# Optimization experiments

Hardware: AMD Instinct MI355X
Metric: run time of the kernel (lower is better)

Reference implementation:

```python
import jax, jax.numpy as jnp
import numpy as np

DELTA_VAR = 0.5
DELTA_DIST = 1.5
LOSS_WEIGHT = 1.0
L_MAX = 17  # segment ids 0..16 (0 = background)
EPS = 1e-12


def setup_inputs() -> dict:
    key = jax.random.key(0)
    k1, k2 = jax.random.split(key)
    B, D, H, W = 16, 16, 288, 512
    emb = jax.random.normal(k1, (B, D, H, W), dtype=jnp.float32)
    seg = jax.random.randint(k2, (B, 1, H, W), 0, L_MAX, dtype=jnp.int64)
    return {"input": emb, "target": seg}


def _per_image_losses(e, s):
    # e: [D, N] float, s: [N] int labels in [0, L_MAX)
    D, N = e.shape
    et = e.T  # [N, D]
    cnt = jax.ops.segment_sum(jnp.ones((N,), e.dtype), s, num_segments=L_MAX)  # [L]
    sums = jax.ops.segment_sum(et, s, num_segments=L_MAX)                      # [L, D]
    present = (cnt > 0) & (jnp.arange(L_MAX) != 0)
    num_lanes = jnp.sum(present).astype(e.dtype)
    means = sums / jnp.maximum(cnt, 1.0)[:, None]                              # [L, D]

    # variance (pull) term: per-pixel distance to own-label centroid
    diff = et - means[s]                                                       # [N, D]
    nrm = jnp.sqrt(jnp.maximum(jnp.sum(diff * diff, axis=1), EPS))             # [N]
    term = jax.nn.relu(nrm - DELTA_VAR) ** 2
    per_label = jax.ops.segment_sum(term, s, num_segments=L_MAX) / jnp.maximum(cnt, 1.0)
    var_l = jnp.sum(jnp.where(present, per_label, 0.0)) / jnp.maximum(num_lanes, 1.0)
    var_l = jnp.where(num_lanes > 0, var_l, 0.0)

    # distance (push) term: pairwise centroid distances among present lanes
    d = means[:, None, :] - means[None, :, :]                                  # [L, L, D]
    sumsq = jnp.sum(d * d, axis=2)                                             # [L, L]
    pair_mask = present[:, None] & present[None, :] & ~jnp.eye(L_MAX, dtype=bool)
    dist = jnp.sqrt(jnp.where(pair_mask, sumsq, 1.0))
    push = jnp.sum(jnp.where(pair_mask, jax.nn.relu(DELTA_DIST - dist) ** 2, 0.0))
    denom = jnp.maximum(num_lanes * (num_lanes - 1.0), 1.0)
    dist_l = jnp.where(num_lanes > 1, push / denom / 2.0, 0.0)
    return var_l, dist_l


def reference(input, target):
    B, D, H, W = input.shape
    N = H * W
    emb = input.reshape(B, D, N)
    seg = target.reshape(B, N).astype(jnp.int32)
    var_l, dist_l = jax.vmap(_per_image_losses)(emb, seg)
    loss = (jnp.sum(var_l) + jnp.sum(dist_l)) / B
    return loss * LOSS_WEIGHT
```

## Files before the change

kernel.cpp:

```cpp
#include <hip/hip_runtime.h>

#define BB   16
#define DD   16
#define NN   (288*512)
#define LL   17
#define TPB  256
#define PB   96
#define QB   (NN/4/PB)
#define PBV  144
#define NREP 8

#define FSCALE 32768.0f
#define INV_FSCALE (1.0f/32768.0f)


__global__ __launch_bounds__(TPB) void k_accum(const float* __restrict__ emb,
                                               const int* __restrict__ seg,
                                               int* __restrict__ acc) {
    __shared__ int tab[NREP * 289];
    const int tid  = threadIdx.x;
    const int b    = blockIdx.y;
    const int blk  = blockIdx.x;
    const int dgrp = tid >> 6;
    const int j    = tid & 63;
    int* trep = tab + (j & (NREP - 1)) * 289;

    for (int i = tid; i < NREP * 289; i += TPB) tab[i] = 0;

    const float* embb = emb + (size_t)b * DD * NN;
    const int*   segb = seg + (size_t)b * NN;
    const float* r0 = embb + (size_t)(dgrp * 4 + 0) * NN;
    const float* r1 = embb + (size_t)(dgrp * 4 + 1) * NN;
    const float* r2 = embb + (size_t)(dgrp * 4 + 2) * NN;
    const float* r3 = embb + (size_t)(dgrp * 4 + 3) * NN;
    const int q0 = blk * QB;
    __syncthreads();

#pragma unroll
    for (int it = 0; it < QB / 64; ++it) {
        const int n = (q0 + it * 64 + j) * 4;
        const int4   s4 = *(const int4*)(segb + n);
        const float4 e0 = *(const float4*)(r0 + n);
        const float4 e1 = *(const float4*)(r1 + n);
        const float4 e2 = *(const float4*)(r2 + n);
        const float4 e3 = *(const float4*)(r3 + n);
        const int ch = dgrp * 4;
        const int o0 = s4.x * 17 + ch;
        const int o1 = s4.y * 17 + ch;
        const int o2 = s4.z * 17 + ch;
        const int o3 = s4.w * 17 + ch;
        atomicAdd(trep + o0 + 0, __float2int_rn(e0.x * FSCALE));
        atomicAdd(trep + o0 + 1, __float2int_rn(e1.x * FSCALE));
        atomicAdd(trep + o0 + 2, __float2int_rn(e2.x * FSCALE));
        atomicAdd(trep + o0 + 3, __float2int_rn(e3.x * FSCALE));
        atomicAdd(trep + o1 + 0, __float2int_rn(e0.y * FSCALE));
        atomicAdd(trep + o1 + 1, __float2int_rn(e1.y * FSCALE));
        atomicAdd(trep + o1 + 2, __float2int_rn(e2.y * FSCALE));
        atomicAdd(trep + o1 + 3, __float2int_rn(e3.y * FSCALE));
        atomicAdd(trep + o2 + 0, __float2int_rn(e0.z * FSCALE));
        atomicAdd(trep + o2 + 1, __float2int_rn(e1.z * FSCALE));
        atomicAdd(trep + o2 + 2, __float2int_rn(e2.z * FSCALE));
        atomicAdd(trep + o2 + 3, __float2int_rn(e3.z * FSCALE));
        atomicAdd(trep + o3 + 0, __float2int_rn(e0.w * FSCALE));
        atomicAdd(trep + o3 + 1, __float2int_rn(e1.w * FSCALE));
        atomicAdd(trep + o3 + 2, __float2int_rn(e2.w * FSCALE));
        atomicAdd(trep + o3 + 3, __float2int_rn(e3.w * FSCALE));
        if (dgrp == 0) {
            atomicAdd(trep + s4.x * 17 + 16, 1);
            atomicAdd(trep + s4.y * 17 + 16, 1);
            atomicAdd(trep + s4.z * 17 + 16, 1);
            atomicAdd(trep + s4.w * 17 + 16, 1);
        }
    }
    __syncthreads();

    for (int i = tid; i < 289; i += TPB) {
        int v = 0;
#pragma unroll
        for (int r = 0; r < NREP; ++r) v += tab[r * 289 + i];
        atomicAdd(acc + b * 289 + i, v);
    }
}

__global__ __launch_bounds__(TPB) void k_var(const float* __restrict__ emb,
                                             const int* __restrict__ seg,
                                             const int* __restrict__ acc,
                                             float* __restrict__ vpart) {
    __shared__ float m[289];
    __shared__ float wl[17];
    __shared__ float wsum[TPB / 64];
    const int tid = threadIdx.x;
    const int b = blockIdx.y;

    for (int i = tid; i < 289; i += TPB) {
        const int raw = acc[b * 289 + i];
        m[i] = (i % 17 == 16) ? (float)raw : (float)raw * INV_FSCALE;
    }
    __syncthreads();
    for (int i = tid; i < 272; i += TPB) {
        const int l = i >> 4, d = i & 15;
        m[l * 17 + d] /= fmaxf(m[l * 17 + 16], 1.f);
    }
    __syncthreads();

    int nl = 0;
#pragma unroll
    for (int l = 1; l < LL; ++l) nl += (m[l * 17 + 16] > 0.f) ? 1 : 0;
    const float nlf = (float)nl;
    if (tid < LL) {
        const bool pres = (tid != 0) && (m[tid * 17 + 16] > 0.f);
        wl[tid] = pres ? 1.f / (fmaxf(m[tid * 17 + 16], 1.f) * fmaxf(nlf, 1.f) * (float)BB)
                       : 0.f;
    }
    __syncthreads();

    const float* embb = emb + (size_t)b * DD * NN;
    const int*   segb = seg + (size_t)b * NN;

    const int n = blockIdx.x * (TPB * 4) + tid * 4;
    const int4 s4 = *(const int4*)(segb + n);
    const int o0 = s4.x * 17, o1 = s4.y * 17, o2 = s4.z * 17, o3 = s4.w * 17;
    float ss0 = 0.f, ss1 = 0.f, ss2 = 0.f, ss3 = 0.f;
#pragma unroll
    for (int d = 0; d < DD; ++d) {
        const float4 e = *(const float4*)(embb + (size_t)d * NN + n);
        const float d0 = e.x - m[o0 + d]; ss0 += d0 * d0;
        const float d1 = e.y - m[o1 + d]; ss1 += d1 * d1;
        const float d2 = e.z - m[o2 + d]; ss2 += d2 * d2;
        const float d3 = e.w - m[o3 + d]; ss3 += d3 * d3;
    }
    float accl = 0.f, t;
    t = fmaxf(sqrtf(fmaxf(ss0, 1e-12f)) - 0.5f, 0.f); accl += t * t * wl[s4.x];
    t = fmaxf(sqrtf(fmaxf(ss1, 1e-12f)) - 0.5f, 0.f); accl += t * t * wl[s4.y];
    t = fmaxf(sqrtf(fmaxf(ss2, 1e-12f)) - 0.5f, 0.f); accl += t * t * wl[s4.z];
    t = fmaxf(sqrtf(fmaxf(ss3, 1e-12f)) - 0.5f, 0.f); accl += t * t * wl[s4.w];

    if (blockIdx.x == 0 && nl > 1) {
        float push = 0.f;
        for (int p = tid; p < 289; p += TPB) {
            const int i = p / 17, jj = p % 17;
            if (i != jj && i > 0 && jj > 0 && m[i*17+16] > 0.f && m[jj*17+16] > 0.f) {
                float ss = 0.f;
#pragma unroll
                for (int d = 0; d < DD; ++d) {
                    const float df = m[i*17+d] - m[jj*17+d];
                    ss += df * df;
                }
                const float u = fmaxf(1.5f - sqrtf(ss), 0.f);
                push += u * u;
            }
        }
        accl += push / (fmaxf(nlf * (nlf - 1.f), 1.f) * 2.f * (float)BB);
    }

#pragma unroll
    for (int off = 32; off; off >>= 1) accl += __shfl_down(accl, off, 64);
    if ((tid & 63) == 0) wsum[tid >> 6] = accl;
    __syncthreads();
    if (tid == 0)
        vpart[(size_t)b * PBV + blockIdx.x] = wsum[0] + wsum[1] + wsum[2] + wsum[3];
}

__global__ __launch_bounds__(TPB) void k_final(const float* __restrict__ vpart,
                                               float* __restrict__ out) {
    __shared__ float ws4[TPB / 64];
    float v = 0.f;
    for (int i = threadIdx.x; i < BB * PBV; i += TPB) v += vpart[i];
#pragma unroll
    for (int off = 32; off; off >>= 1) v += __shfl_down(v, off, 64);
    if ((threadIdx.x & 63) == 0) ws4[threadIdx.x >> 6] = v;
    __syncthreads();
    if (threadIdx.x == 0) out[0] = ws4[0] + ws4[1] + ws4[2] + ws4[3];
}

extern "C" void kernel_launch(void* const* d_in, const int* in_sizes, int n_in,
                              void* d_out, int out_size, void* d_ws, size_t ws_size,
                              hipStream_t stream) {
    const float* emb = (const float*)d_in[0];
    const int*   seg = (const int*)d_in[1];
    float* out = (float*)d_out;

    int*   acc   = (int*)d_ws;
    float* vpart = (float*)(acc + BB * 289);

    hipMemsetAsync(acc, 0, (size_t)BB * 289 * sizeof(int), stream);

    k_accum<<<dim3(PB, BB), TPB, 0, stream>>>(emb, seg, acc);
    k_var  <<<dim3(PBV, BB), TPB, 0, stream>>>(emb, seg, acc, vpart);
    k_final<<<1, TPB, 0, stream>>>(vpart, out);
}
```

Measured before the change: 246.2 us.

## Fuse accumulate, variance and final reduce into one cooperative kernel with grid sync

Adds a cooperative kernel that runs centroid accumulation, a grid-wide sync, the variance/push pass and the final reduction in one launch. Each block processes the same pixel range in both phases, so the second read of the embeddings may hit the large last-level cache instead of HBM. Launch overhead for three kernels is also removed. The cost is lower occupancy (512 blocks of 256 threads), grid-sync latency, and dependence on cooperative launch support, with the old three-kernel path kept as a fallback.

```diff
diff --git a/kernel.cpp b/kernel.cpp
--- a/kernel.cpp
+++ b/kernel.cpp
@@ -1,29 +1,46 @@
 #include <hip/hip_runtime.h>
+#include <hip/hip_cooperative_groups.h>
+
+namespace cg = cooperative_groups;
 
 #define BB   16
 #define DD   16
 #define NN   (288*512)
 #define LL   17
 #define TPB  256
+#define NREP 8
+
+#define NBLK 512
+#define BPI  (NBLK/BB)
+#define PXB  (NN/BPI)
+#define QB   (PXB/4)
+
 #define PB   96
-#define QB   (NN/4/PB)
+#define QBF  (NN/4/PB)
 #define PBV  144
-#define NREP 8
 
 #define FSCALE 32768.0f
 #define INV_FSCALE (1.0f/32768.0f)
 
 
-__global__ __launch_bounds__(TPB) void k_accum(const float* __restrict__ emb,
-                                               const int* __restrict__ seg,
-                                               int* __restrict__ acc) {
-    __shared__ int tab[NREP * 289];
+__global__ __launch_bounds__(TPB, 2) void k_fused(const float* __restrict__ emb,
+                                                  const int* __restrict__ seg,
+                                                  int* __restrict__ acc,
+                                                  float* __restrict__ vpart,
+                                                  float* __restrict__ out) {
+    __shared__ int   tab[NREP * 289];
+    __shared__ float m[289];
+    __shared__ float wl[LL];
+    __shared__ float wsum[TPB / 64];
+
+    cg::grid_group grid = cg::this_grid();
+
     const int tid  = threadIdx.x;
-    const int b    = blockIdx.y;
-    const int blk  = blockIdx.x;
+    const int bid  = blockIdx.x;
+    const int b    = bid / BPI;
+    const int blk  = bid % BPI;
     const int dgrp = tid >> 6;
     const int j    = tid & 63;
-    int* trep = tab + (j & (NREP - 1)) * 289;
 
     for (int i = tid; i < NREP * 289; i += TPB) tab[i] = 0;
 
@@ -34,9 +51,9 @@
     const float* r2 = embb + (size_t)(dgrp * 4 + 2) * NN;
     const float* r3 = embb + (size_t)(dgrp * 4 + 3) * NN;
     const int q0 = blk * QB;
-    __syncthreads();
-
-#pragma unroll
+    int* trep = tab + (j & (NREP - 1)) * 289;
+    __syncthreads();
+
     for (int it = 0; it < QB / 64; ++it) {
         const int n = (q0 + it * 64 + j) * 4;
         const int4   s4 = *(const int4*)(segb + n);
@@ -73,6 +90,155 @@
         }
     }
     __syncthreads();
+    for (int i = tid; i < 289; i += TPB) {
+        int v = 0;
+#pragma unroll
+        for (int r = 0; r < NREP; ++r) v += tab[r * 289 + i];
+        atomicAdd(acc + b * 289 + i, v);
+    }
+
+    grid.sync();
+
+    for (int i = tid; i < 289; i += TPB) {
+        const int raw = acc[b * 289 + i];
+        m[i] = (i % 17 == 16) ? (float)raw : (float)raw * INV_FSCALE;
+    }
+    __syncthreads();
+    for (int i = tid; i < 272; i += TPB) {
+        const int l = i >> 4, d = i & 15;
+        m[l * 17 + d] /= fmaxf(m[l * 17 + 16], 1.f);
+    }
+    __syncthreads();
+
+    int nl = 0;
+#pragma unroll
+    for (int l = 1; l < LL; ++l) nl += (m[l * 17 + 16] > 0.f) ? 1 : 0;
+    const float nlf = (float)nl;
+    if (tid < LL) {
+        const bool pres = (tid != 0) && (m[tid * 17 + 16] > 0.f);
+        wl[tid] = pres ? 1.f / (fmaxf(m[tid * 17 + 16], 1.f) * fmaxf(nlf, 1.f) * (float)BB)
+                       : 0.f;
+    }
+    __syncthreads();
+
+    float accl = 0.f;
+    const int base = blk * PXB;
+    for (int p = tid * 4; p < PXB; p += TPB * 4) {
+        const int n = base + p;
+        const int4 s4 = *(const int4*)(segb + n);
+        const int o0 = s4.x * 17, o1 = s4.y * 17, o2 = s4.z * 17, o3 = s4.w * 17;
+        float ss0 = 0.f, ss1 = 0.f, ss2 = 0.f, ss3 = 0.f;
+#pragma unroll
+        for (int d = 0; d < DD; ++d) {
+            const float4 e = *(const float4*)(embb + (size_t)d * NN + n);
+            const float d0 = e.x - m[o0 + d]; ss0 += d0 * d0;
+            const float d1 = e.y - m[o1 + d]; ss1 += d1 * d1;
+            const float d2 = e.z - m[o2 + d]; ss2 += d2 * d2;
+            const float d3 = e.w - m[o3 + d]; ss3 += d3 * d3;
+        }
+        float t;
+        t = fmaxf(sqrtf(fmaxf(ss0, 1e-12f)) - 0.5f, 0.f); accl += t * t * wl[s4.x];
+        t = fmaxf(sqrtf(fmaxf(ss1, 1e-12f)) - 0.5f, 0.f); accl += t * t * wl[s4.y];
+        t = fmaxf(sqrtf(fmaxf(ss2, 1e-12f)) - 0.5f, 0.f); accl += t * t * wl[s4.z];
+        t = fmaxf(sqrtf(fmaxf(ss3, 1e-12f)) - 0.5f, 0.f); accl += t * t * wl[s4.w];
+    }
+
+    if (blk == 0 && nl > 1) {
+        float push = 0.f;
+        for (int p = tid; p < 289; p += TPB) {
+            const int i = p / 17, jj = p % 17;
+            if (i != jj && i > 0 && jj > 0 && m[i*17+16] > 0.f && m[jj*17+16] > 0.f) {
+                float ss = 0.f;
+#pragma unroll
+                for (int d = 0; d < DD; ++d) {
+                    const float df = m[i*17+d] - m[jj*17+d];
+                    ss += df * df;
+                }
+                const float u = fmaxf(1.5f - sqrtf(ss), 0.f);
+                push += u * u;
+            }
+        }
+        accl += push / (fmaxf(nlf * (nlf - 1.f), 1.f) * 2.f * (float)BB);
+    }
+
+#pragma unroll
+    for (int off = 32; off; off >>= 1) accl += __shfl_down(accl, off, 64);
+    if ((tid & 63) == 0) wsum[tid >> 6] = accl;
+    __syncthreads();
+    if (tid == 0) vpart[bid] = wsum[0] + wsum[1] + wsum[2] + wsum[3];
+
+    grid.sync();
+
+    if (bid == 0) {
+        float v = 0.f;
+        for (int i = tid; i < NBLK; i += TPB) v += vpart[i];
+#pragma unroll
+        for (int off = 32; off; off >>= 1) v += __shfl_down(v, off, 64);
+        if ((tid & 63) == 0) wsum[tid >> 6] = v;
+        __syncthreads();
+        if (tid == 0) out[0] = wsum[0] + wsum[1] + wsum[2] + wsum[3];
+    }
+}
+
+__global__ __launch_bounds__(TPB) void k_accum(const float* __restrict__ emb,
+                                               const int* __restrict__ seg,
+                                               int* __restrict__ acc) {
+    __shared__ int tab[NREP * 289];
+    const int tid  = threadIdx.x;
+    const int b    = blockIdx.y;
+    const int blk  = blockIdx.x;
+    const int dgrp = tid >> 6;
+    const int j    = tid & 63;
+    int* trep = tab + (j & (NREP - 1)) * 289;
+
+    for (int i = tid; i < NREP * 289; i += TPB) tab[i] = 0;
+
+    const float* embb = emb + (size_t)b * DD * NN;
+    const int*   segb = seg + (size_t)b * NN;
+    const float* r0 = embb + (size_t)(dgrp * 4 + 0) * NN;
+    const float* r1 = embb + (size_t)(dgrp * 4 + 1) * NN;
+    const float* r2 = embb + (size_t)(dgrp * 4 + 2) * NN;
+    const float* r3 = embb + (size_t)(dgrp * 4 + 3) * NN;
+    const int q0 = blk * QBF;
+    __syncthreads();
+
+#pragma unroll
+    for (int it = 0; it < QBF / 64; ++it) {
+        const int n = (q0 + it * 64 + j) * 4;
+        const int4   s4 = *(const int4*)(segb + n);
+        const float4 e0 = *(const float4*)(r0 + n);
+        const float4 e1 = *(const float4*)(r1 + n);
+        const float4 e2 = *(const float4*)(r2 + n);
+        const float4 e3 = *(const float4*)(r3 + n);
+        const int ch = dgrp * 4;
+        const int o0 = s4.x * 17 + ch;
+        const int o1 = s4.y * 17 + ch;
+        const int o2 = s4.z * 17 + ch;
+        const int o3 = s4.w * 17 + ch;
+        atomicAdd(trep + o0 + 0, __float2int_rn(e0.x * FSCALE));
+        atomicAdd(trep + o0 + 1, __float2int_rn(e1.x * FSCALE));
+        atomicAdd(trep + o0 + 2, __float2int_rn(e2.x * FSCALE));
+        atomicAdd(trep + o0 + 3, __float2int_rn(e3.x * FSCALE));
+        atomicAdd(trep + o1 + 0, __float2int_rn(e0.y * FSCALE));
+        atomicAdd(trep + o1 + 1, __float2int_rn(e1.y * FSCALE));
+        atomicAdd(trep + o1 + 2, __float2int_rn(e2.y * FSCALE));
+        atomicAdd(trep + o1 + 3, __float2int_rn(e3.y * FSCALE));
+        atomicAdd(trep + o2 + 0, __float2int_rn(e0.z * FSCALE));
+        atomicAdd(trep + o2 + 1, __float2int_rn(e1.z * FSCALE));
+        atomicAdd(trep + o2 + 2, __float2int_rn(e2.z * FSCALE));
+        atomicAdd(trep + o2 + 3, __float2int_rn(e3.z * FSCALE));
+        atomicAdd(trep + o3 + 0, __float2int_rn(e0.w * FSCALE));
+        atomicAdd(trep + o3 + 1, __float2int_rn(e1.w * FSCALE));
+        atomicAdd(trep + o3 + 2, __float2int_rn(e2.w * FSCALE));
+        atomicAdd(trep + o3 + 3, __float2int_rn(e3.w * FSCALE));
+        if (dgrp == 0) {
+            atomicAdd(trep + s4.x * 17 + 16, 1);
+            atomicAdd(trep + s4.y * 17 + 16, 1);
+            atomicAdd(trep + s4.z * 17 + 16, 1);
+            atomicAdd(trep + s4.w * 17 + 16, 1);
+        }
+    }
+    __syncthreads();
 
     for (int i = tid; i < 289; i += TPB) {
         int v = 0;
@@ -185,6 +351,19 @@
 
     hipMemsetAsync(acc, 0, (size_t)BB * 289 * sizeof(int), stream);
 
+    int maxb = 0;
+    hipError_t qerr = hipOccupancyMaxActiveBlocksPerMultiprocessor(
+        &maxb, (const void*)k_fused, TPB, 0);
+    bool coop = (qerr == hipSuccess) && (maxb * 256 >= NBLK);
+
+    if (coop) {
+        void* args[] = {(void*)&emb, (void*)&seg, (void*)&acc, (void*)&vpart, (void*)&out};
+        hipError_t lerr = hipLaunchCooperativeKernel((const void*)k_fused, dim3(NBLK),
+                                                     dim3(TPB), args, 0, stream);
+        if (lerr == hipSuccess) return;
+        (void)hipGetLastError();
+    }
+
     k_accum<<<dim3(PB, BB), TPB, 0, stream>>>(emb, seg, acc);
     k_var  <<<dim3(PBV, BB), TPB, 0, stream>>>(emb, seg, acc, vpart);
     k_final<<<1, TPB, 0, stream>>>(vpart, out);
```

New measurement: 365.4 us. 48.4% more time.
